# Kernel tuning notes

Hardware: AMD Instinct MI355X
Metric: run time of the kernel (lower is better)

The kernel has to match this reference:

```python
import jax, jax.numpy as jnp
import numpy as np

N_VARS = 512
K = 32
B = 192
LOG2PI = 1.8378770664093453


def setup_inputs() -> dict:
    key = jax.random.key(0)
    k1, k2, k3, k4, k5 = jax.random.split(key, 5)
    X = jax.random.normal(k1, (B, N_VARS), dtype=jnp.float32)
    # one-hot cluster assignment matrix C: [n_vars, k]
    assign = jax.random.randint(k2, (N_VARS,), 0, K)
    C = jax.nn.one_hot(assign, K, dtype=jnp.float32)
    # cluster-level adjacency G: [k, k], binary
    G = (jax.random.uniform(k3, (K, K)) < 0.3).astype(jnp.float32)
    W = jax.random.normal(k4, (N_VARS, N_VARS), dtype=jnp.float32) / np.sqrt(N_VARS).astype(np.float32)
    b = jax.random.normal(k5, (N_VARS,), dtype=jnp.float32) * 0.01
    sigma = jnp.array([0.1], dtype=jnp.float32)
    rho = jnp.array([0.99], dtype=jnp.float32)
    return dict(X=X, C=C, G=G, W=W, b=b, sigma=sigma, rho=rho)


def reference(X, C, G, W, b, sigma, rho):
    n = X.shape[1]
    # expand cluster adjacency to variable-level mask: [n, n]
    G_expand = C @ G @ C.T
    # MaskedLinear: F.linear(X, W * mask, b)
    mean = X @ (W * G_expand).T + b  # [B, n]
    # cluster-structured covariance: sigma^2 * ((1-rho) I + rho * C C^T)
    M = C @ C.T  # same-cluster indicator (incl. diagonal)
    Cov = (sigma[0] ** 2) * ((1.0 - rho[0]) * jnp.eye(n, dtype=X.dtype) + rho[0] * M)
    L = jnp.linalg.cholesky(Cov)
    # torch MVN broadcasting: value [B,1,n] vs loc [B,n] -> log_prob [B,B]
    diff = X[:, None, :] - mean[None, :, :]  # [B, B, n]
    nb = diff.shape[0] * diff.shape[1]
    rhs = diff.reshape(nb, n).T  # [n, B*B]
    y = jax.scipy.linalg.solve_triangular(L, rhs, lower=True)  # [n, B*B]
    maha = jnp.sum(y * y, axis=0)  # [B*B]
    logdet = 2.0 * jnp.sum(jnp.log(jnp.diagonal(L)))
    logp = -0.5 * (maha + logdet + n * LOG2PI)
    return logp.mean()
```

## Files before the change

### kernel.cpp

```cpp
#include <hip/hip_runtime.h>
#include <math.h>

#define NV 512
#define KC 32
#define NB 192
#define LOG2PI 1.8378770664093453f

#define WS_G 0
#define G_STRIDE 1088
#define WS_S 104448
#define S_STRIDE 608
#define WS_P 119040

__global__ __launch_bounds__(256) void partial_kernel(
    const float* __restrict__ X, const float* __restrict__ C,
    const float* __restrict__ G, const float* __restrict__ W,
    const float* __restrict__ bias, const float* __restrict__ sigma,
    const float* __restrict__ rho, float* __restrict__ wsF)
{
    const int bid = blockIdx.x, tid = threadIdx.x;
    __shared__ int asg[NV];
    __shared__ float Gs[KC * KC];
    __shared__ float XsT[32][34];
    __shared__ float WsT[32][34];
    __shared__ float smtile[32 * KC];
    __shared__ float varr[32];
    __shared__ float redw[8];
    __shared__ float smrows[8][KC];

    for (int n = tid; n < NV; n += 256) {
        const float* row = C + n * KC;
        float a = 0.f;
        #pragma unroll
        for (int c = 0; c < KC; ++c) a += row[c] * (float)c;
        asg[n] = (int)(a + 0.5f);
    }

    if (bid < 96) {
        for (int l = tid; l < KC * KC; l += 256) Gs[l] = G[l];
        for (int l = tid; l < 32 * KC; l += 256) smtile[l] = 0.f;
        if (tid < 32) varr[tid] = 0.f;
        if (tid < 8) redw[tid] = 0.f;
        __syncthreads();
        const int i0 = (bid & 15) * 32, b0 = (bid >> 4) * 32;
        const int tx = tid & 15, ty = tid >> 4;
        float a00 = 0.f, a01 = 0.f, a10 = 0.f, a11 = 0.f;
        for (int kt = 0; kt < 16; ++kt) {
            const int k0 = kt * 32;
            #pragma unroll
            for (int p = 0; p < 4; ++p) {
                const int l = tid + p * 256;
                const int r2 = l >> 5, c2 = l & 31;
                XsT[c2][r2] = X[(b0 + r2) * NV + k0 + c2];
                WsT[c2][r2] = W[(i0 + r2) * NV + k0 + c2]
                            * Gs[asg[i0 + r2] * KC + asg[k0 + c2]];
            }
            __syncthreads();
            #pragma unroll
            for (int kk = 0; kk < 32; ++kk) {
                const float2 xv = *(const float2*)&XsT[kk][ty * 2];
                const float2 wv = *(const float2*)&WsT[kk][tx * 2];
                a00 += xv.x * wv.x; a01 += xv.x * wv.y;
                a10 += xv.y * wv.x; a11 += xv.y * wv.y;
            }
            __syncthreads();
        }
        const int col0 = i0 + tx * 2, col1 = col0 + 1;
        const float bf0 = bias[col0], bf1 = bias[col1];
        const int ci0 = asg[col0], ci1 = asg[col1];
        const int r0 = ty * 2, r1 = r0 + 1;
        const float v00 = a00 + bf0, v01 = a01 + bf1;
        const float v10 = a10 + bf0, v11 = a11 + bf1;
        float mml = v00 * v00 + v01 * v01 + v10 * v10 + v11 * v11;
        atomicAdd(&smtile[r0 * KC + ci0], v00);
        atomicAdd(&smtile[r0 * KC + ci1], v01);
        atomicAdd(&smtile[r1 * KC + ci0], v10);
        atomicAdd(&smtile[r1 * KC + ci1], v11);
        atomicAdd(&varr[tx * 2], v00 + v10);
        atomicAdd(&varr[tx * 2 + 1], v01 + v11);
        for (int off = 32; off; off >>= 1) mml += __shfl_down(mml, off, 64);
        if ((tid & 63) == 0) redw[tid >> 6] = mml;
        __syncthreads();
        float* slice = wsF + WS_G + bid * G_STRIDE;
        for (int l = tid; l < 32 * KC; l += 256) slice[l] = smtile[l];
        if (tid < 32) slice[1024 + tid] = varr[tid];
        if (tid == 0) slice[1056] = redw[0] + redw[1] + redw[2] + redw[3];
    } else if (bid < 120) {
        for (int l = tid; l < 8 * KC; l += 256) ((float*)smrows)[l] = 0.f;
        if (tid < 8) redw[tid] = 0.f;
        __syncthreads();
        const int sb = bid - 96, row0 = sb * 8;
        const int c0 = tid * 2;
        const int ca = asg[c0], cb = asg[c0 + 1];
        float u0 = 0.f, u1 = 0.f, xx = 0.f;
        #pragma unroll
        for (int r = 0; r < 8; ++r) {
            const float2 xv = *(const float2*)(X + (row0 + r) * NV + c0);
            u0 += xv.x; u1 += xv.y;
            xx += xv.x * xv.x + xv.y * xv.y;
            atomicAdd(&smrows[r][ca], xv.x);
            atomicAdd(&smrows[r][cb], xv.y);
        }
        for (int off = 32; off; off >>= 1) xx += __shfl_down(xx, off, 64);
        if ((tid & 63) == 0) redw[tid >> 6] = xx;
        __syncthreads();
        float* slice = wsF + WS_S + sb * S_STRIDE;
        slice[c0] = u0; slice[c0 + 1] = u1;
        if (tid < KC) {
            float s1 = 0.f, s2 = 0.f;
            #pragma unroll
            for (int r = 0; r < 8; ++r) { const float s = smrows[r][tid]; s1 += s; s2 += s * s; }
            slice[512 + tid] = s1;
            slice[544 + tid] = s2;
        }
        if (tid == 0) slice[576] = redw[0] + redw[1] + redw[2] + redw[3];
    } else {
        __shared__ int cnt[KC];
        __shared__ float ldred[KC];
        if (tid < KC) cnt[tid] = 0;
        __syncthreads();
        for (int n = tid; n < NV; n += 256) atomicAdd(&cnt[asg[n]], 1);
        __syncthreads();
        const float s2v = sigma[0] * sigma[0], rh = rho[0];
        const float av = s2v * (1.f - rh), bv = s2v * rh;
        if (tid < KC) {
            const int nc = cnt[tid];
            wsF[WS_P + tid] = bv / (av * (av + bv * (float)nc));
            ldred[tid] = (float)(nc - 1) * logf(av) + logf(av + bv * (float)nc);
        }
        __syncthreads();
        if (tid == 0) {
            float ld = 0.f;
            for (int c = 0; c < KC; ++c) ld += ldred[c];
            wsF[WS_P + 32] = ld;
        }
    }
}

__global__ __launch_bounds__(512) void finalize_kernel(
    const float* __restrict__ sigma, const float* __restrict__ rho,
    const float* __restrict__ wsF, float* __restrict__ out)
{
    const int tid = threadIdx.x;
    __shared__ float SM1s[KC], SM2s[KC];
    __shared__ float accs[4];
    if (tid < KC) { SM1s[tid] = 0.f; SM2s[tid] = 0.f; }
    if (tid < 4) accs[tid] = 0.f;
    __syncthreads();
    const float* gS = wsF + WS_G;
    const float* sS = wsF + WS_S;
    #pragma unroll
    for (int w = 0; w < 12; ++w) {
        const int o = tid + w * 512;
        const int b = o >> 5, c = o & 31;
        const float* p = gS + (b >> 5) * 16 * G_STRIDE + (b & 31) * KC + c;
        float s = 0.f;
        #pragma unroll
        for (int it = 0; it < 16; ++it) s += p[it * G_STRIDE];
        atomicAdd(&SM1s[c], s);
        atomicAdd(&SM2s[c], s * s);
    }
    {
        const int i = tid;
        const int it = i >> 5;
        float v = 0.f;
        #pragma unroll
        for (int bt = 0; bt < 6; ++bt) v += gS[(bt * 16 + it) * G_STRIDE + 1024 + (i & 31)];
        float u = 0.f;
        #pragma unroll
        for (int sb = 0; sb < 24; ++sb) u += sS[sb * S_STRIDE + i];
        float cr = u * v;
        for (int off = 32; off; off >>= 1) cr += __shfl_down(cr, off, 64);
        if ((tid & 63) == 0) atomicAdd(&accs[2], cr);
    }
    {
        float mm = (tid < 96) ? gS[tid * G_STRIDE + 1056] : 0.f;
        for (int off = 32; off; off >>= 1) mm += __shfl_down(mm, off, 64);
        if ((tid & 63) == 0) atomicAdd(&accs[0], mm);
    }
    {
        float xx = (tid < 24) ? sS[tid * S_STRIDE + 576] : 0.f;
        for (int off = 32; off; off >>= 1) xx += __shfl_down(xx, off, 64);
        if ((tid & 63) == 0) atomicAdd(&accs[1], xx);
    }
    __syncthreads();
    float qv = 0.f;
    if (tid < KC) {
        float s1 = 0.f, s2 = 0.f;
        #pragma unroll
        for (int sb = 0; sb < 24; ++sb) {
            s1 += sS[sb * S_STRIDE + 512 + tid];
            s2 += sS[sb * S_STRIDE + 544 + tid];
        }
        const float coef = wsF[WS_P + tid];
        qv = coef * (s2 * (1.f / NB) + SM2s[tid] * (1.f / NB)
                     - 2.f * s1 * SM1s[tid] * (1.f / ((float)NB * (float)NB)));
    }
    for (int off = 16; off; off >>= 1) qv += __shfl_down(qv, off, 64);
    if (tid == 0) atomicAdd(&accs[3], qv);
    __syncthreads();
    if (tid == 0) {
        const float s2v = sigma[0] * sigma[0], rh = rho[0];
        const float av = s2v * (1.f - rh);
        const float meanD2 = accs[1] * (1.f / NB) + accs[0] * (1.f / NB)
                           - 2.f * accs[2] / ((float)NB * (float)NB);
        const float maha = meanD2 / av - accs[3];
        out[0] = -0.5f * (maha + wsF[WS_P + 32] + (float)NV * LOG2PI);
    }
}

extern "C" void kernel_launch(void* const* d_in, const int* in_sizes, int n_in,
                              void* d_out, int out_size, void* d_ws, size_t ws_size,
                              hipStream_t stream) {
    const float* X     = (const float*)d_in[0];
    const float* C     = (const float*)d_in[1];
    const float* G     = (const float*)d_in[2];
    const float* W     = (const float*)d_in[3];
    const float* b     = (const float*)d_in[4];
    const float* sigma = (const float*)d_in[5];
    const float* rho   = (const float*)d_in[6];
    float* wsF = (float*)d_ws;
    float* out = (float*)d_out;

    hipLaunchKernelGGL(partial_kernel, dim3(121), dim3(256), 0, stream,
                       X, C, G, W, b, sigma, rho, wsF);
    hipLaunchKernelGGL(finalize_kernel, dim3(1), dim3(512), 0, stream,
                       sigma, rho, wsF, out);
}
```

Before: 106.7 us.

## Split into prep, bf16 MFMA GEMM, and finalize kernels

Moves the masked W·X GEMM from a scalar fp32 LDS-tiled loop to bf16 MFMA 16x16x32 instructions. A new prep kernel converts X and the masked W to bf16 in workspace, and cluster sums are accumulated with global atomics instead of per-block slices. This adds a third launch and a workspace round trip, and bf16 rounding may reduce accuracy of the mean.

Measured after the change: 86.87 us. 18.6% less time.

```diff
diff --git a/kernel.cpp b/kernel.cpp
--- a/kernel.cpp
+++ b/kernel.cpp
@@ -6,27 +6,34 @@
 #define NB 192
 #define LOG2PI 1.8378770664093453f
 
-#define WS_G 0
-#define G_STRIDE 1088
-#define WS_S 104448
-#define S_STRIDE 608
-#define WS_P 119040
-
-__global__ __launch_bounds__(256) void partial_kernel(
+typedef __attribute__((ext_vector_type(8))) short short8;
+typedef __attribute__((ext_vector_type(4))) float float4v;
+
+#define WS_SM    0
+#define WS_GV    6144
+#define WS_STATS 12400
+#define WS_P     27000
+#define WS_ASG   27040
+#define WS_XBF   27552
+#define WS_WBF   76704
+
+static __device__ inline ushort f2bf(float f) {
+    uint u = __float_as_uint(f);
+    uint r = (u + 0x7fffu + ((u >> 16) & 1u)) >> 16;
+    return (ushort)r;
+}
+
+__global__ __launch_bounds__(256) void prep_kernel(
     const float* __restrict__ X, const float* __restrict__ C,
     const float* __restrict__ G, const float* __restrict__ W,
     const float* __restrict__ bias, const float* __restrict__ sigma,
-    const float* __restrict__ rho, float* __restrict__ wsF)
+    const float* __restrict__ rho, float* __restrict__ wsF, int* __restrict__ wsI)
 {
     const int bid = blockIdx.x, tid = threadIdx.x;
     __shared__ int asg[NV];
     __shared__ float Gs[KC * KC];
-    __shared__ float XsT[32][34];
-    __shared__ float WsT[32][34];
-    __shared__ float smtile[32 * KC];
-    __shared__ float varr[32];
-    __shared__ float redw[8];
     __shared__ float smrows[8][KC];
+    __shared__ float redw[4];
 
     for (int n = tid; n < NV; n += 256) {
         const float* row = C + n * KC;
@@ -36,60 +43,41 @@
         asg[n] = (int)(a + 0.5f);
     }
 
-    if (bid < 96) {
+    if (bid < 24) {
+        __syncthreads();
+        ushort* xbf = (ushort*)(wsF + WS_XBF);
+        const int base = bid * 8 * NV;
+        #pragma unroll
+        for (int p = 0; p < 4; ++p) {
+            const int off = base + tid * 4 + p * 1024;
+            const float4 f = *(const float4*)(X + off);
+            ushort4 o;
+            o.x = f2bf(f.x); o.y = f2bf(f.y); o.z = f2bf(f.z); o.w = f2bf(f.w);
+            *(ushort4*)(xbf + off) = o;
+        }
+    } else if (bid < 88) {
         for (int l = tid; l < KC * KC; l += 256) Gs[l] = G[l];
-        for (int l = tid; l < 32 * KC; l += 256) smtile[l] = 0.f;
-        if (tid < 32) varr[tid] = 0.f;
-        if (tid < 8) redw[tid] = 0.f;
-        __syncthreads();
-        const int i0 = (bid & 15) * 32, b0 = (bid >> 4) * 32;
-        const int tx = tid & 15, ty = tid >> 4;
-        float a00 = 0.f, a01 = 0.f, a10 = 0.f, a11 = 0.f;
-        for (int kt = 0; kt < 16; ++kt) {
-            const int k0 = kt * 32;
-            #pragma unroll
-            for (int p = 0; p < 4; ++p) {
-                const int l = tid + p * 256;
-                const int r2 = l >> 5, c2 = l & 31;
-                XsT[c2][r2] = X[(b0 + r2) * NV + k0 + c2];
-                WsT[c2][r2] = W[(i0 + r2) * NV + k0 + c2]
-                            * Gs[asg[i0 + r2] * KC + asg[k0 + c2]];
-            }
-            __syncthreads();
-            #pragma unroll
-            for (int kk = 0; kk < 32; ++kk) {
-                const float2 xv = *(const float2*)&XsT[kk][ty * 2];
-                const float2 wv = *(const float2*)&WsT[kk][tx * 2];
-                a00 += xv.x * wv.x; a01 += xv.x * wv.y;
-                a10 += xv.y * wv.x; a11 += xv.y * wv.y;
-            }
-            __syncthreads();
-        }
-        const int col0 = i0 + tx * 2, col1 = col0 + 1;
-        const float bf0 = bias[col0], bf1 = bias[col1];
-        const int ci0 = asg[col0], ci1 = asg[col1];
-        const int r0 = ty * 2, r1 = r0 + 1;
-        const float v00 = a00 + bf0, v01 = a01 + bf1;
-        const float v10 = a10 + bf0, v11 = a11 + bf1;
-        float mml = v00 * v00 + v01 * v01 + v10 * v10 + v11 * v11;
-        atomicAdd(&smtile[r0 * KC + ci0], v00);
-        atomicAdd(&smtile[r0 * KC + ci1], v01);
-        atomicAdd(&smtile[r1 * KC + ci0], v10);
-        atomicAdd(&smtile[r1 * KC + ci1], v11);
-        atomicAdd(&varr[tx * 2], v00 + v10);
-        atomicAdd(&varr[tx * 2 + 1], v01 + v11);
-        for (int off = 32; off; off >>= 1) mml += __shfl_down(mml, off, 64);
-        if ((tid & 63) == 0) redw[tid >> 6] = mml;
-        __syncthreads();
-        float* slice = wsF + WS_G + bid * G_STRIDE;
-        for (int l = tid; l < 32 * KC; l += 256) slice[l] = smtile[l];
-        if (tid < 32) slice[1024 + tid] = varr[tid];
-        if (tid == 0) slice[1056] = redw[0] + redw[1] + redw[2] + redw[3];
-    } else if (bid < 120) {
+        __syncthreads();
+        ushort* wbf = (ushort*)(wsF + WS_WBF);
+        const int i0 = (bid - 24) * 8;
+        #pragma unroll
+        for (int p = 0; p < 4; ++p) {
+            const int l = tid * 4 + p * 1024;
+            const int ir = i0 + (l >> 9), k = l & 511;
+            const float* grow = Gs + asg[ir] * KC;
+            const float4 f = *(const float4*)(W + ir * NV + k);
+            ushort4 o;
+            o.x = f2bf(f.x * grow[asg[k]]);
+            o.y = f2bf(f.y * grow[asg[k + 1]]);
+            o.z = f2bf(f.z * grow[asg[k + 2]]);
+            o.w = f2bf(f.w * grow[asg[k + 3]]);
+            *(ushort4*)(wbf + ir * NV + k) = o;
+        }
+    } else if (bid < 112) {
         for (int l = tid; l < 8 * KC; l += 256) ((float*)smrows)[l] = 0.f;
-        if (tid < 8) redw[tid] = 0.f;
-        __syncthreads();
-        const int sb = bid - 96, row0 = sb * 8;
+        if (tid < 4) redw[tid] = 0.f;
+        __syncthreads();
+        const int sb = bid - 88, row0 = sb * 8;
         const int c0 = tid * 2;
         const int ca = asg[c0], cb = asg[c0 + 1];
         float u0 = 0.f, u1 = 0.f, xx = 0.f;
@@ -104,7 +92,7 @@
         for (int off = 32; off; off >>= 1) xx += __shfl_down(xx, off, 64);
         if ((tid & 63) == 0) redw[tid >> 6] = xx;
         __syncthreads();
-        float* slice = wsF + WS_S + sb * S_STRIDE;
+        float* slice = wsF + WS_STATS + sb * 608;
         slice[c0] = u0; slice[c0 + 1] = u1;
         if (tid < KC) {
             float s1 = 0.f, s2 = 0.f;
@@ -119,7 +107,11 @@
         __shared__ float ldred[KC];
         if (tid < KC) cnt[tid] = 0;
         __syncthreads();
-        for (int n = tid; n < NV; n += 256) atomicAdd(&cnt[asg[n]], 1);
+        for (int n = tid; n < NV; n += 256) {
+            atomicAdd(&cnt[asg[n]], 1);
+            wsI[WS_ASG + n] = asg[n];
+        }
+        for (int l = tid; l < NB * KC; l += 256) wsF[WS_SM + l] = 0.f;
         __syncthreads();
         const float s2v = sigma[0] * sigma[0], rh = rho[0];
         const float av = s2v * (1.f - rh), bv = s2v * rh;
@@ -137,7 +129,61 @@
     }
 }
 
-__global__ __launch_bounds__(512) void finalize_kernel(
+__global__ __launch_bounds__(256) void gemm_kernel(
+    const float* __restrict__ bias, float* __restrict__ wsF, const int* __restrict__ wsI)
+{
+    const int bid = blockIdx.x, tid = threadIdx.x;
+    const int blk_b = bid >> 3, blk_i = bid & 7;
+    const int b0 = blk_b * 16, i0blk = blk_i * 64;
+    const int w = tid >> 6, lane = tid & 63;
+    const int m = lane & 15, q = lane >> 4;
+    const int i0w = i0blk + w * 16;
+
+    __shared__ float smL[16 * KC];
+    __shared__ float varr[64];
+    __shared__ int asgc[64];
+    __shared__ float mmred[4];
+    for (int l = tid; l < 16 * KC; l += 256) smL[l] = 0.f;
+    if (tid < 64) { varr[tid] = 0.f; asgc[tid] = wsI[WS_ASG + i0blk + tid]; }
+    if (tid < 4) mmred[tid] = 0.f;
+
+    const ushort* xbf = (const ushort*)(wsF + WS_XBF);
+    const ushort* wbf = (const ushort*)(wsF + WS_WBF);
+    const short8* ap = (const short8*)(xbf + (b0 + m) * NV + q * 8);
+    const short8* bp = (const short8*)(wbf + (i0w + m) * NV + q * 8);
+    float4v acc = {0.f, 0.f, 0.f, 0.f};
+    #pragma unroll
+    for (int s = 0; s < 16; ++s) {
+        const short8 a = ap[s * 4];
+        const short8 b = bp[s * 4];
+        acc = __builtin_amdgcn_mfma_f32_16x16x32_bf16(a, b, acc, 0, 0, 0);
+    }
+    __syncthreads();
+
+    const int col = i0w + m;
+    const float bv = bias[col];
+    const int ca = asgc[w * 16 + m];
+    float vsum = 0.f, mml = 0.f;
+    #pragma unroll
+    for (int r = 0; r < 4; ++r) {
+        const float val = acc[r] + bv;
+        vsum += val; mml += val * val;
+        atomicAdd(&smL[(q * 4 + r) * KC + ca], val);
+    }
+    atomicAdd(&varr[w * 16 + m], vsum);
+    for (int off = 32; off; off >>= 1) mml += __shfl_down(mml, off, 64);
+    if (lane == 0) mmred[w] = mml;
+    __syncthreads();
+
+    float* smG = wsF + WS_SM;
+    for (int l = tid; l < 16 * KC; l += 256)
+        atomicAdd(&smG[(b0 + (l >> 5)) * KC + (l & 31)], smL[l]);
+    float* slice = wsF + WS_GV + bid * 65;
+    if (tid < 64) slice[tid] = varr[tid];
+    if (tid == 0) slice[64] = mmred[0] + mmred[1] + mmred[2] + mmred[3];
+}
+
+__global__ __launch_bounds__(256) void finalize_kernel(
     const float* __restrict__ sigma, const float* __restrict__ rho,
     const float* __restrict__ wsF, float* __restrict__ out)
 {
@@ -147,57 +193,65 @@
     if (tid < KC) { SM1s[tid] = 0.f; SM2s[tid] = 0.f; }
     if (tid < 4) accs[tid] = 0.f;
     __syncthreads();
-    const float* gS = wsF + WS_G;
-    const float* sS = wsF + WS_S;
-    #pragma unroll
-    for (int w = 0; w < 12; ++w) {
-        const int o = tid + w * 512;
-        const int b = o >> 5, c = o & 31;
-        const float* p = gS + (b >> 5) * 16 * G_STRIDE + (b & 31) * KC + c;
-        float s = 0.f;
-        #pragma unroll
-        for (int it = 0; it < 16; ++it) s += p[it * G_STRIDE];
-        atomicAdd(&SM1s[c], s);
-        atomicAdd(&SM2s[c], s * s);
-    }
-    {
-        const int i = tid;
-        const int it = i >> 5;
-        float v = 0.f;
-        #pragma unroll
-        for (int bt = 0; bt < 6; ++bt) v += gS[(bt * 16 + it) * G_STRIDE + 1024 + (i & 31)];
-        float u = 0.f;
-        #pragma unroll
-        for (int sb = 0; sb < 24; ++sb) u += sS[sb * S_STRIDE + i];
-        float cr = u * v;
+    const float* sm = wsF + WS_SM;
+    const float* gv = wsF + WS_GV;
+    const float* st = wsF + WS_STATS;
+
+    {
+        const int c = tid & 31, r0 = tid >> 5;
+        float s1 = 0.f, s2 = 0.f;
+        #pragma unroll
+        for (int j = 0; j < 24; ++j) {
+            const float s = sm[(r0 + 8 * j) * KC + c];
+            s1 += s; s2 += s * s;
+        }
+        atomicAdd(&SM1s[c], s1);
+        atomicAdd(&SM2s[c], s2);
+    }
+    {
+        float cr = 0.f;
+        #pragma unroll
+        for (int h = 0; h < 2; ++h) {
+            const int i = tid + h * 256;
+            float u = 0.f;
+            #pragma unroll
+            for (int sb = 0; sb < 24; ++sb) u += st[sb * 608 + i];
+            float v = 0.f;
+            const int blk_i = i >> 6, loc = i & 63;
+            #pragma unroll
+            for (int bb = 0; bb < 12; ++bb) v += gv[(bb * 8 + blk_i) * 65 + loc];
+            cr += u * v;
+        }
         for (int off = 32; off; off >>= 1) cr += __shfl_down(cr, off, 64);
         if ((tid & 63) == 0) atomicAdd(&accs[2], cr);
     }
     {
-        float mm = (tid < 96) ? gS[tid * G_STRIDE + 1056] : 0.f;
+        float mm = (tid < 96) ? gv[tid * 65 + 64] : 0.f;
         for (int off = 32; off; off >>= 1) mm += __shfl_down(mm, off, 64);
         if ((tid & 63) == 0) atomicAdd(&accs[0], mm);
     }
     {
-        float xx = (tid < 24) ? sS[tid * S_STRIDE + 576] : 0.f;
+        float xx = (tid < 24) ? st[tid * 608 + 576] : 0.f;
         for (int off = 32; off; off >>= 1) xx += __shfl_down(xx, off, 64);
         if ((tid & 63) == 0) atomicAdd(&accs[1], xx);
     }
     __syncthreads();
-    float qv = 0.f;
-    if (tid < KC) {
-        float s1 = 0.f, s2 = 0.f;
-        #pragma unroll
-        for (int sb = 0; sb < 24; ++sb) {
-            s1 += sS[sb * S_STRIDE + 512 + tid];
-            s2 += sS[sb * S_STRIDE + 544 + tid];
-        }
-        const float coef = wsF[WS_P + tid];
-        qv = coef * (s2 * (1.f / NB) + SM2s[tid] * (1.f / NB)
-                     - 2.f * s1 * SM1s[tid] * (1.f / ((float)NB * (float)NB)));
-    }
-    for (int off = 16; off; off >>= 1) qv += __shfl_down(qv, off, 64);
-    if (tid == 0) atomicAdd(&accs[3], qv);
+    {
+        float qv = 0.f;
+        if (tid < KC) {
+            float s1 = 0.f, s2 = 0.f;
+            #pragma unroll
+            for (int sb = 0; sb < 24; ++sb) {
+                s1 += st[sb * 608 + 512 + tid];
+                s2 += st[sb * 608 + 544 + tid];
+            }
+            const float coef = wsF[WS_P + tid];
+            qv = coef * (s2 * (1.f / NB) + SM2s[tid] * (1.f / NB)
+                         - 2.f * s1 * SM1s[tid] * (1.f / ((float)NB * (float)NB)));
+        }
+        for (int off = 32; off; off >>= 1) qv += __shfl_down(qv, off, 64);
+        if (tid == 0) atomicAdd(&accs[3], qv);
+    }
     __syncthreads();
     if (tid == 0) {
         const float s2v = sigma[0] * sigma[0], rh = rho[0];
@@ -220,10 +274,13 @@
     const float* sigma = (const float*)d_in[5];
     const float* rho   = (const float*)d_in[6];
     float* wsF = (float*)d_ws;
+    int*   wsI = (int*)d_ws;
     float* out = (float*)d_out;
 
-    hipLaunchKernelGGL(partial_kernel, dim3(121), dim3(256), 0, stream,
-                       X, C, G, W, b, sigma, rho, wsF);
-    hipLaunchKernelGGL(finalize_kernel, dim3(1), dim3(512), 0, stream,
+    hipLaunchKernelGGL(prep_kernel, dim3(113), dim3(256), 0, stream,
+                       X, C, G, W, b, sigma, rho, wsF, wsI);
+    hipLaunchKernelGGL(gemm_kernel, dim3(96), dim3(256), 0, stream,
+                       b, wsF, wsI);
+    hipLaunchKernelGGL(finalize_kernel, dim3(1), dim3(256), 0, stream,
                        sigma, rho, wsF, out);
 }
```
